# Kernel tuning notes

Hardware: AMD Instinct MI355X
Metric: run time of the kernel (lower is better)

The kernel has to match this reference:

```python
import jax, jax.numpy as jnp
import numpy as np

H, T, E = 8, 2048, 512


def setup_inputs() -> dict:
    key = jax.random.key(0)
    ks = jax.random.split(key, 11)
    s_e = 1.0 / np.sqrt(E)
    s_f = 1.0 / np.sqrt(H * T)
    return {
        "x": jax.random.normal(ks[0], (T, E), jnp.float32),
        "y": jax.random.normal(ks[1], (T, E), jnp.float32),
        "z": jax.random.normal(ks[2], (T, E), jnp.float32),
        "Wq": jax.random.normal(ks[3], (H, E, E), jnp.float32) * s_e,
        "bq": jax.random.normal(ks[4], (H, E), jnp.float32) * s_e,
        "Wk": jax.random.normal(ks[5], (H, E, E), jnp.float32) * s_e,
        "bk": jax.random.normal(ks[6], (H, E), jnp.float32) * s_e,
        "Wv": jax.random.normal(ks[7], (H, E, E), jnp.float32) * s_e,
        "bv": jax.random.normal(ks[8], (H, E), jnp.float32) * s_e,
        "Wf": jax.random.normal(ks[9], (T, H * T), jnp.float32) * s_f,
        "bf": jax.random.normal(ks[10], (T,), jnp.float32) * s_f,
    }


def reference(x, y, z, Wq, bq, Wk, bk, Wv, bv, Wf, bf):
    # Per-head projections: torch Linear is x @ W.T + b, W is [out,in]
    q = jnp.einsum("se,hfe->hsf", x, Wq) + bq[:, None, :]  # [H,T,E]
    k = jnp.einsum("se,hfe->hsf", y, Wk) + bk[:, None, :]
    v = jnp.einsum("se,hfe->hsf", z, Wv) + bv[:, None, :]
    # Scores scaled by sqrt(num query rows) = sqrt(T), as in the source
    scores = jnp.einsum("hsf,htf->hst", q, k) / jnp.sqrt(jnp.asarray(T, x.dtype))
    att = jax.nn.softmax(scores, axis=-1)
    heads_out = jnp.einsum("hst,htf->hsf", att, v)  # [H,T,E]
    concat = heads_out.reshape(H * T, E)  # cat along dim 0
    # finalLinear applied to concat.T: [E, H*T] @ Wf.T -> [E, T], then transpose
    final = (concat.T @ Wf.T + bf).T  # [T, E]
    residual = final + z
    # Manual per-row LayerNorm: (x - mean) / sqrt(std^2 + 1e-4), population std
    mean = jnp.mean(residual, axis=1, keepdims=True)
    var = jnp.var(residual, axis=1, keepdims=True)
    return (residual - mean) / jnp.sqrt(var + 1e-4)
```

## Files before the change

### kernel.cpp

```cpp
#include <hip/hip_runtime.h>
#include <hip/hip_bf16.h>
#include <cstdint>


#define HH 8
#define TT 2048
#define EE 512
#define HT (HH * TT)
#define HE (HH * EE)

typedef __bf16 bf16_t;
typedef __attribute__((ext_vector_type(8))) __bf16 bf16x8;
typedef __attribute__((ext_vector_type(4))) float f32x4;

__device__ __forceinline__ void gld_lds16(const bf16_t* __restrict__ g, bf16_t* l) {
  __builtin_amdgcn_global_load_lds(
      (const __attribute__((address_space(1))) unsigned int*)g,
      (__attribute__((address_space(3))) unsigned int*)l, 16, 0, 0);
}

__device__ __forceinline__ bf16x8 cvt8(float4 u, float4 v) {
  bf16x8 o;
  o[0] = (__bf16)u.x; o[1] = (__bf16)u.y; o[2] = (__bf16)u.z; o[3] = (__bf16)u.w;
  o[4] = (__bf16)v.x; o[5] = (__bf16)v.y; o[6] = (__bf16)v.z; o[7] = (__bf16)v.w;
  return o;
}

#define XCD_SWIZZLE()                                                              \
  const int gx = gridDim.x, gy = gridDim.y;                                        \
  const int nwg = gx * gy * (int)gridDim.z;                                        \
  const int lin = blockIdx.x + gx * (blockIdx.y + gy * blockIdx.z);                \
  const int qn_ = nwg >> 3, rn_ = nwg & 7;                                         \
  const int xcd_ = lin & 7, sub_ = lin >> 3;                                       \
  const int wgid =                                                                 \
      (xcd_ < rn_ ? xcd_ * (qn_ + 1) : rn_ * (qn_ + 1) + (xcd_ - rn_) * qn_) + sub_; \
  const int bx = wgid % gx;                                                        \
  const int t1_ = wgid / gx;                                                       \
  const int by = t1_ % gy;                                                         \
  const int z = t1_ / gy;

template <typename CT>
__global__ __launch_bounds__(512, 2) void gemm256_8ph(
    const bf16_t* __restrict__ A, const bf16_t* __restrict__ B, CT* __restrict__ C,
    const float* __restrict__ bias_n,
    int K, int lda, int ldb, int ldc,
    int64_t sA, int64_t sB, int64_t sC, int64_t sBN) {
  XCD_SWIZZLE();
  A += z * sA;
  B += z * sB;
  C += z * sC;
  if (bias_n) bias_n += z * sBN;

  const int m0 = bx * 256;
  const int n0 = by * 256;
  const int tid = threadIdx.x;

  __shared__ bf16_t lds[65536];
  bf16_t* sAl = lds;
  bf16_t* sBl = lds + 32768;

  const int srow = tid >> 3;
  const int csw = ((tid & 7) ^ (srow & 7)) * 8;
  const bf16_t* aS = A + (int64_t)(m0 + srow) * lda + csw;
  const bf16_t* bS = B + (int64_t)(n0 + srow) * ldb + csw;
  const int64_t l64a = (int64_t)64 * lda, l64b = (int64_t)64 * ldb;

  const int wave = tid >> 6, lane = tid & 63;
  const int wr = wave >> 2, wc = wave & 3;
  const int fr = lane & 15, qd = lane >> 4;
  const int aoff = wr * 8192 + fr * 64;
  const int boff = wc * 4096 + fr * 64;
  const int ck0 = ((0 * 4 + qd) ^ (fr & 7)) * 8;
  const int ck1 = ((1 * 4 + qd) ^ (fr & 7)) * 8;

  f32x4 acc[8][4];
#pragma unroll
  for (int i = 0; i < 8; i++)
#pragma unroll
    for (int j = 0; j < 4; j++) acc[i][j] = (f32x4){0.f, 0.f, 0.f, 0.f};

  bf16x8 aR[2][8];
  bf16x8 bR[2][2];

#define STG_A(d, h, t)                                                        \
  do {                                                                        \
    const bf16_t* g_ = aS + (int64_t)(h) * 128 * lda + (int64_t)(t) * 64;     \
    gld_lds16(g_, &sAl[(d) * 16384 + (h) * 8192 + tid * 8]);                  \
    gld_lds16(g_ + l64a, &sAl[(d) * 16384 + (h) * 8192 + 4096 + tid * 8]);    \
  } while (0)
#define STG_B(d, h, t)                                                        \
  do {                                                                        \
    const bf16_t* g_ = bS + (int64_t)(h) * 128 * ldb + (int64_t)(t) * 64;     \
    gld_lds16(g_, &sBl[(d) * 16384 + (h) * 8192 + tid * 8]);                  \
    gld_lds16(g_ + l64b, &sBl[(d) * 16384 + (h) * 8192 + 4096 + tid * 8]);    \
  } while (0)
#define RD_A(d, ih)                                                           \
  _Pragma("unroll") for (int i_ = 0; i_ < 4; i_++) {                          \
    const int b_ = (d) * 16384 + aoff + ((ih) * 4 + i_) * 1024;               \
    aR[0][(ih) * 4 + i_] = *(const bf16x8*)&sAl[b_ + ck0];                    \
    aR[1][(ih) * 4 + i_] = *(const bf16x8*)&sAl[b_ + ck1];                    \
  }
#define RD_B(d, jh)                                                           \
  _Pragma("unroll") for (int j_ = 0; j_ < 2; j_++) {                          \
    const int b_ = (d) * 16384 + boff + ((jh) * 2 + j_) * 1024;               \
    bR[0][j_] = *(const bf16x8*)&sBl[b_ + ck0];                               \
    bR[1][j_] = *(const bf16x8*)&sBl[b_ + ck1];                               \
  }
#define MM(qm, qn)                                                            \
  do {                                                                        \
    __builtin_amdgcn_s_setprio(1);                                            \
    _Pragma("unroll") for (int ks = 0; ks < 2; ks++)                          \
        _Pragma("unroll") for (int i_ = 0; i_ < 4; i_++)                      \
            _Pragma("unroll") for (int j_ = 0; j_ < 2; j_++)                  \
                acc[(qm) * 4 + i_][(qn) * 2 + j_] =                           \
                    __builtin_amdgcn_mfma_f32_16x16x32_bf16(                  \
                        aR[ks][(qm) * 4 + i_], bR[ks][j_],                    \
                        acc[(qm) * 4 + i_][(qn) * 2 + j_], 0, 0, 0);          \
    __builtin_amdgcn_s_setprio(0);                                            \
  } while (0)
#define BAR __builtin_amdgcn_s_barrier()
#define LGKM0                                                                 \
  do {                                                                        \
    asm volatile("s_waitcnt lgkmcnt(0)" ::: "memory");                        \
    __builtin_amdgcn_sched_barrier(0);                                        \
  } while (0)
#define VMC(n)                                                                \
  do {                                                                        \
    asm volatile("s_waitcnt vmcnt(" #n ")" ::: "memory");                     \
    __builtin_amdgcn_sched_barrier(0);                                        \
  } while (0)

  const int NT = K >> 6;

  STG_A(0, 0, 0); STG_A(0, 1, 0); STG_B(0, 0, 0); STG_B(0, 1, 0);
  STG_A(1, 0, 1); STG_A(1, 1, 1);
  VMC(4);
  BAR;

  for (int t0 = 0; t0 < NT; t0 += 2) {
    const int t1 = t0 + 1;
    const bool m2 = (t0 + 2) < NT;
    RD_A(0, 0); RD_B(0, 0);
    STG_B(1, 0, t1);
    BAR; LGKM0; MM(0, 0); BAR;
    RD_A(0, 1);
    STG_B(1, 1, t1);
    BAR; LGKM0; MM(1, 0); BAR;
    RD_B(0, 1);
    if (m2) STG_A(0, 0, t0 + 2);
    BAR; LGKM0; MM(0, 1); BAR;
    if (m2) STG_A(0, 1, t0 + 2);
    BAR; MM(1, 1);
    if (m2) { VMC(4); } else { VMC(0); }
    BAR;
    RD_A(1, 0); RD_B(1, 0);
    if (m2) STG_B(0, 0, t0 + 2);
    BAR; LGKM0; MM(0, 0); BAR;
    RD_A(1, 1);
    if (m2) STG_B(0, 1, t0 + 2);
    BAR; LGKM0; MM(1, 0); BAR;
    RD_B(1, 1);
    if (m2) STG_A(1, 0, t1 + 2);
    BAR; LGKM0; MM(0, 1); BAR;
    if (m2) STG_A(1, 1, t1 + 2);
    BAR; MM(1, 1);
    if (m2) VMC(4);
    BAR;
  }

#undef STG_A
#undef STG_B
#undef RD_A
#undef RD_B
#undef MM
#undef BAR
#undef LGKM0
#undef VMC

#pragma unroll
  for (int i = 0; i < 8; i++) {
    const int row0 = m0 + wr * 128 + i * 16 + qd * 4;
#pragma unroll
    for (int j = 0; j < 4; j++) {
      const int col = n0 + wc * 64 + j * 16 + fr;
      const float bn = bias_n ? bias_n[col] : 0.f;
#pragma unroll
      for (int r = 0; r < 4; r++)
        C[(int64_t)(row0 + r) * ldc + col] = (CT)(acc[i][j][r] + bn);
    }
  }
}

template <typename AT, typename CT>
__global__ __launch_bounds__(512, 4) void mfma_gemm_nt(
    const AT* __restrict__ A, const bf16_t* __restrict__ B, CT* __restrict__ C,
    const float* __restrict__ bias_m, const float* __restrict__ bias_n,
    int K, int lda, int ldb, int ldc,
    int64_t sA, int64_t sB, int64_t sC, int64_t sBM, int64_t sBN) {
  XCD_SWIZZLE();
  A += z * sA;
  B += z * sB;
  C += z * sC;
  if (bias_m) bias_m += z * sBM;
  if (bias_n) bias_n += z * sBN;

  const int m0 = bx * 128;
  const int n0 = by * 128;
  const int tid = threadIdx.x;

  __shared__ bf16_t sAb[2][128 * 64];
  __shared__ bf16_t sBb[2][128 * 64];

  const int srow = tid >> 3;
  const int sc = tid & 7;
  const int csw = (sc ^ (srow & 7)) * 8;
  const AT* a0 = A + (int64_t)(m0 + srow) * lda + csw;
  const AT* a1 = a0 + (int64_t)64 * lda;
  const bf16_t* b0 = B + (int64_t)(n0 + srow) * ldb + csw;
  const bf16_t* b1 = b0 + (int64_t)64 * ldb;

  const int wave = tid >> 6;
  const int lane = tid & 63;
  const int wm = (wave >> 2) * 64;
  const int wn = (wave & 3) * 32;
  const int fr = lane & 15;
  const int qd = lane >> 4;
  const int cx0 = ((0 * 4 + qd) ^ (fr & 7)) * 8;
  const int cx1 = ((1 * 4 + qd) ^ (fr & 7)) * 8;

  f32x4 acc[4][2];
#pragma unroll
  for (int i = 0; i < 4; i++)
#pragma unroll
    for (int j = 0; j < 2; j++) acc[i][j] = (f32x4){0.f, 0.f, 0.f, 0.f};

  float4 pa[4];

#define STAGE_B(buf, kt)                              \
  do {                                                \
    gld_lds16(b0 + (kt), &sBb[buf][tid * 8]);         \
    gld_lds16(b1 + (kt), &sBb[buf][4096 + tid * 8]);  \
  } while (0)
#define STAGE_A_BF16(buf, kt)                         \
  do {                                                \
    gld_lds16(a0 + (kt), &sAb[buf][tid * 8]);         \
    gld_lds16(a1 + (kt), &sAb[buf][4096 + tid * 8]);  \
  } while (0)
#define LOAD_A_F32(kt)                                \
  do {                                                \
    pa[0] = ((const float4*)(a0 + (kt)))[0];          \
    pa[1] = ((const float4*)(a0 + (kt)))[1];          \
    pa[2] = ((const float4*)(a1 + (kt)))[0];          \
    pa[3] = ((const float4*)(a1 + (kt)))[1];          \
  } while (0)
#define WRITE_A_F32(buf)                                      \
  do {                                                        \
    *(bf16x8*)&sAb[buf][tid * 8] = cvt8(pa[0], pa[1]);        \
    *(bf16x8*)&sAb[buf][4096 + tid * 8] = cvt8(pa[2], pa[3]); \
  } while (0)
#define COMPUTE(buf)                                                                   \
  do {                                                                                 \
    bf16x8 af[2][4], bfr[2][2];                                                        \
    _Pragma("unroll") for (int i = 0; i < 4; i++) {                                    \
      const int ar = (wm + i * 16 + fr) * 64;                                          \
      af[0][i] = *(const bf16x8*)&sAb[buf][ar + cx0];                                  \
      af[1][i] = *(const bf16x8*)&sAb[buf][ar + cx1];                                  \
    }                                                                                  \
    _Pragma("unroll") for (int j = 0; j < 2; j++) {                                    \
      const int br = (wn + j * 16 + fr) * 64;                                          \
      bfr[0][j] = *(const bf16x8*)&sBb[buf][br + cx0];                                 \
      bfr[1][j] = *(const bf16x8*)&sBb[buf][br + cx1];                                 \
    }                                                                                  \
    _Pragma("unroll") for (int ks = 0; ks < 2; ks++)                                   \
        _Pragma("unroll") for (int i = 0; i < 4; i++)                                  \
            _Pragma("unroll") for (int j = 0; j < 2; j++)                              \
                acc[i][j] = __builtin_amdgcn_mfma_f32_16x16x32_bf16(                   \
                    af[ks][i], bfr[ks][j], acc[i][j], 0, 0, 0);                        \
  } while (0)

  if constexpr (sizeof(AT) == 2) {
    STAGE_A_BF16(0, 0);
  } else {
    LOAD_A_F32(0);
    WRITE_A_F32(0);
  }
  STAGE_B(0, 0);
  __syncthreads();

  for (int kt = 0; kt < K; kt += 128) {
    if constexpr (sizeof(AT) == 2) {
      STAGE_A_BF16(1, kt + 64);
    } else {
      LOAD_A_F32(kt + 64);
    }
    STAGE_B(1, kt + 64);
    COMPUTE(0);
    if constexpr (sizeof(AT) == 4) WRITE_A_F32(1);
    __syncthreads();

    const bool more = (kt + 128) < K;
    if (more) {
      if constexpr (sizeof(AT) == 2) {
        STAGE_A_BF16(0, kt + 128);
      } else {
        LOAD_A_F32(kt + 128);
      }
      STAGE_B(0, kt + 128);
    }
    COMPUTE(1);
    if constexpr (sizeof(AT) == 4) {
      if (more) WRITE_A_F32(0);
    }
    __syncthreads();
  }

#undef STAGE_B
#undef STAGE_A_BF16
#undef LOAD_A_F32
#undef WRITE_A_F32
#undef COMPUTE

#pragma unroll
  for (int i = 0; i < 4; i++) {
    const int row0 = m0 + wm + i * 16 + qd * 4;
#pragma unroll
    for (int j = 0; j < 2; j++) {
      const int col = n0 + wn + j * 16 + fr;
      const float bn = bias_n ? bias_n[col] : 0.f;
#pragma unroll
      for (int r = 0; r < 4; r++) {
        const float bm = bias_m ? bias_m[row0 + r] : 0.f;
        C[(int64_t)(row0 + r) * ldc + col] = (CT)(acc[i][j][r] + bn + bm);
      }
    }
  }
}

__global__ __launch_bounds__(256) void fused_cvt(
    const float* __restrict__ x, const float* __restrict__ y,
    const float* __restrict__ z, const float* __restrict__ Wq,
    const float* __restrict__ Wk, const float* __restrict__ Wv,
    bf16_t* __restrict__ xb, bf16_t* __restrict__ yb, bf16_t* __restrict__ zb,
    bf16_t* __restrict__ Wqb, bf16_t* __restrict__ Wkb, bf16_t* __restrict__ Wvb) {
  const int b = blockIdx.x;
  const float* s;
  bf16_t* d;
  int off;
  if (b < 512) { s = x; d = xb; off = b; }
  else if (b < 1024) { s = y; d = yb; off = b - 512; }
  else if (b < 1536) { s = z; d = zb; off = b - 1024; }
  else if (b < 2560) { s = Wq; d = Wqb; off = b - 1536; }
  else if (b < 3584) { s = Wk; d = Wkb; off = b - 2560; }
  else { s = Wv; d = Wvb; off = b - 3584; }
  const int64_t i = ((int64_t)off * 256 + threadIdx.x) * 8;
  float4 u = ((const float4*)(s + i))[0];
  float4 v = ((const float4*)(s + i))[1];
  *(bf16x8*)(d + i) = cvt8(u, v);
}

__global__ __launch_bounds__(256) void softmax_rows(bf16_t* __restrict__ S) {
  const float scale = 0.022097086912079608f;
  bf16_t* p = S + (int64_t)blockIdx.x * TT;
  const int tid = threadIdx.x;
  bf16x8 in = *(const bf16x8*)(p + tid * 8);
  float v[8];
  float mx = -1e30f;
#pragma unroll
  for (int i = 0; i < 8; i++) {
    v[i] = (float)in[i] * scale;
    mx = fmaxf(mx, v[i]);
  }
#pragma unroll
  for (int o = 32; o > 0; o >>= 1) mx = fmaxf(mx, __shfl_xor(mx, o));
  __shared__ float redm[4], reds[4];
  if ((tid & 63) == 0) redm[tid >> 6] = mx;
  __syncthreads();
  mx = fmaxf(fmaxf(redm[0], redm[1]), fmaxf(redm[2], redm[3]));
  float sum = 0.f;
#pragma unroll
  for (int i = 0; i < 8; i++) {
    v[i] = __expf(v[i] - mx);
    sum += v[i];
  }
#pragma unroll
  for (int o = 32; o > 0; o >>= 1) sum += __shfl_xor(sum, o);
  if ((tid & 63) == 0) reds[tid >> 6] = sum;
  __syncthreads();
  sum = reds[0] + reds[1] + reds[2] + reds[3];
  const float inv = 1.0f / sum;
  bf16x8 o8;
#pragma unroll
  for (int i = 0; i < 8; i++) o8[i] = (__bf16)(v[i] * inv);
  *(bf16x8*)(p + tid * 8) = o8;
}

__global__ __launch_bounds__(256) void ln_res(const float* __restrict__ F,
                                              const float* __restrict__ Z,
                                              const float* __restrict__ BF,
                                              float* __restrict__ O, int np) {
  const int row = blockIdx.x;
  const int tid = threadIdx.x;
  const int64_t off = (int64_t)row * EE + tid;
  float a = 0.f, b = 0.f;
  for (int pz = 0; pz < np; pz++) {
    const float* f = F + (int64_t)pz * TT * EE;
    a += f[off];
    b += f[off + 256];
  }
  const float bft = BF[row];
  a += bft + Z[off];
  b += bft + Z[off + 256];
  float s = a + b, ss = a * a + b * b;
#pragma unroll
  for (int w = 32; w > 0; w >>= 1) {
    s += __shfl_xor(s, w);
    ss += __shfl_xor(ss, w);
  }
  __shared__ float rs[4], rss[4];
  if ((tid & 63) == 0) {
    rs[tid >> 6] = s;
    rss[tid >> 6] = ss;
  }
  __syncthreads();
  s = rs[0] + rs[1] + rs[2] + rs[3];
  ss = rss[0] + rss[1] + rss[2] + rss[3];
  const float mean = s * (1.0f / EE);
  const float var = ss * (1.0f / EE) - mean * mean;
  const float inv = rsqrtf(var + 1e-4f);
  float* o = O + (int64_t)row * EE;
  o[tid] = (a - mean) * inv;
  o[tid + 256] = (b - mean) * inv;
}

extern "C" void kernel_launch(void* const* d_in, const int* in_sizes, int n_in,
                              void* d_out, int out_size, void* d_ws, size_t ws_size,
                              hipStream_t stream) {
  const float* x = (const float*)d_in[0];
  const float* y = (const float*)d_in[1];
  const float* z = (const float*)d_in[2];
  const float* Wq = (const float*)d_in[3];
  const float* bq = (const float*)d_in[4];
  const float* Wk = (const float*)d_in[5];
  const float* bk = (const float*)d_in[6];
  const float* Wv = (const float*)d_in[7];
  const float* bv = (const float*)d_in[8];
  const float* Wf = (const float*)d_in[9];
  const float* bfb = (const float*)d_in[10];
  float* out = (float*)d_out;

  const size_t MB = 1ull << 20;
  char* p = (char*)d_ws;

  if (ws_size >= 151 * MB) {
    bf16_t* xb = (bf16_t*)(p + 0 * MB);
    bf16_t* yb = (bf16_t*)(p + 2 * MB);
    bf16_t* zb = (bf16_t*)(p + 4 * MB);
    bf16_t* Wqb = (bf16_t*)(p + 6 * MB);
    bf16_t* Wkb = (bf16_t*)(p + 10 * MB);
    bf16_t* Wvb = (bf16_t*)(p + 14 * MB);
    bf16_t* q = (bf16_t*)(p + 18 * MB);
    bf16_t* k = (bf16_t*)(p + 34 * MB);
    bf16_t* vT = (bf16_t*)(p + 50 * MB);
    bf16_t* att = (bf16_t*)(p + 66 * MB);
    bf16_t* hoT = (bf16_t*)(p + 130 * MB);
    float* finp = (float*)(p + 66 * MB);

    fused_cvt<<<4608, 256, 0, stream>>>(x, y, z, Wq, Wk, Wv, xb, yb, zb, Wqb, Wkb, Wvb);

    mfma_gemm_nt<bf16_t, bf16_t><<<dim3(16, 32, 1), 512, 0, stream>>>(
        xb, Wqb, q, nullptr, bq, EE, EE, EE, HE, 0, 0, 0, 0, 0);
    mfma_gemm_nt<bf16_t, bf16_t><<<dim3(16, 32, 1), 512, 0, stream>>>(
        yb, Wkb, k, nullptr, bk, EE, EE, EE, HE, 0, 0, 0, 0, 0);
    mfma_gemm_nt<bf16_t, bf16_t><<<dim3(32, 16, 1), 512, 0, stream>>>(
        Wvb, zb, vT, bv, nullptr, EE, EE, EE, TT, 0, 0, 0, 0, 0);
    gemm256_8ph<bf16_t><<<dim3(8, 8, 8), 512, 0, stream>>>(
        q, k, att, nullptr, EE, HE, HE, TT, EE, EE, (int64_t)TT * TT, 0);
    softmax_rows<<<HH * TT, 256, 0, stream>>>(att);
    mfma_gemm_nt<bf16_t, bf16_t><<<dim3(4, 16, 8), 512, 0, stream>>>(
        vT, att, hoT, nullptr, nullptr, TT, TT, TT, HT, (int64_t)EE * TT, (int64_t)TT * TT,
        (int64_t)TT, 0, 0);
    mfma_gemm_nt<float, float><<<dim3(16, 4, 8), 512, 0, stream>>>(
        Wf, hoT, finp, nullptr, nullptr, HT / 8, HT, HT, EE, HT / 8, HT / 8,
        (int64_t)TT * EE, 0, 0);
    ln_res<<<TT, 256, 0, stream>>>(finp, z, bfb, out, 8);
  } else {
    bf16_t* xb = (bf16_t*)(p + 0 * MB);
    bf16_t* yb = (bf16_t*)(p + 2 * MB);
    bf16_t* zb = (bf16_t*)(p + 4 * MB);
    bf16_t* Wqb = (bf16_t*)(p + 6 * MB);
    bf16_t* Wkb = (bf16_t*)(p + 10 * MB);
    bf16_t* Wvb = (bf16_t*)(p + 14 * MB);
    bf16_t* qh = (bf16_t*)(p + 18 * MB);
    bf16_t* kh = (bf16_t*)(p + 20 * MB);
    bf16_t* vTh = (bf16_t*)(p + 22 * MB);
    bf16_t* att = (bf16_t*)(p + 24 * MB);
    bf16_t* hoT = (bf16_t*)(p + 32 * MB);
    float* finp = (float*)(p + 0 * MB);

    fused_cvt<<<4608, 256, 0, stream>>>(x, y, z, Wq, Wk, Wv, xb, yb, zb, Wqb, Wkb, Wvb);

    for (int h = 0; h < HH; h++) {
      const bf16_t* Wq_h = Wqb + (int64_t)h * EE * EE;
      const bf16_t* Wk_h = Wkb + (int64_t)h * EE * EE;
      const bf16_t* Wv_h = Wvb + (int64_t)h * EE * EE;
      mfma_gemm_nt<bf16_t, bf16_t><<<dim3(16, 4, 1), 512, 0, stream>>>(
          xb, Wq_h, qh, nullptr, bq + h * EE, EE, EE, EE, EE, 0, 0, 0, 0, 0);
      mfma_gemm_nt<bf16_t, bf16_t><<<dim3(16, 4, 1), 512, 0, stream>>>(
          yb, Wk_h, kh, nullptr, bk + h * EE, EE, EE, EE, EE, 0, 0, 0, 0, 0);
      mfma_gemm_nt<bf16_t, bf16_t><<<dim3(4, 16, 1), 512, 0, stream>>>(
          Wv_h, zb, vTh, bv + h * EE, nullptr, EE, EE, EE, TT, 0, 0, 0, 0, 0);
      mfma_gemm_nt<bf16_t, bf16_t><<<dim3(16, 16, 1), 512, 0, stream>>>(
          qh, kh, att, nullptr, nullptr, EE, EE, EE, TT, 0, 0, 0, 0, 0);
      softmax_rows<<<TT, 256, 0, stream>>>(att);
      mfma_gemm_nt<bf16_t, bf16_t><<<dim3(4, 16, 1), 512, 0, stream>>>(
          vTh, att, hoT + (int64_t)h * TT, nullptr, nullptr, TT, TT, TT, HT, 0, 0, 0, 0, 0);
    }
    mfma_gemm_nt<float, float><<<dim3(16, 4, 8), 512, 0, stream>>>(
        Wf, hoT, finp, nullptr, nullptr, HT / 8, HT, HT, EE, HT / 8, HT / 8,
        (int64_t)TT * EE, 0, 0);
    ln_res<<<TT, 256, 0, stream>>>(finp, z, bfb, out, 8);
  }
}
```

Measured before the change: 428.3 us.

## Add fp32-A bf16-B k32 GEMM for final linear with 16-way split-K

Replaces the generic mfma_gemm_nt for the final linear with a dedicated kernel. It loads fp32 Wf rows from global memory, converts them to bf16 in registers, stages hoT via direct global-to-LDS loads, and double-buffers 32-wide K tiles. In the main path, split-K goes from 8 to 16 partitions to launch more blocks for this long-K GEMM. This adds more partial outputs for ln_res to sum and more fp32 partial traffic.

```diff
diff --git a/kernel.cpp b/kernel.cpp
--- a/kernel.cpp
+++ b/kernel.cpp
@@ -336,6 +336,102 @@
   }
 }
 
+__global__ __launch_bounds__(512, 8) void gemm_f32a_k32(
+    const float* __restrict__ A, const bf16_t* __restrict__ B, float* __restrict__ C,
+    int K, int lda, int ldb, int ldc, int64_t sA, int64_t sB, int64_t sC) {
+  XCD_SWIZZLE();
+  A += z * sA;
+  B += z * sB;
+  C += z * sC;
+
+  const int m0 = bx * 128;
+  const int n0 = by * 128;
+  const int tid = threadIdx.x;
+
+  __shared__ bf16_t sAb[2][128 * 32];
+  __shared__ bf16_t sBb[2][128 * 32];
+
+  const int srow = tid >> 2;
+  const int csw = ((tid & 3) ^ (srow & 3)) * 8;
+  const float* a0 = A + (int64_t)(m0 + srow) * lda + csw;
+  const bf16_t* b0 = B + (int64_t)(n0 + srow) * ldb + csw;
+
+  const int wave = tid >> 6;
+  const int lane = tid & 63;
+  const int wm = (wave >> 2) * 64;
+  const int wn = (wave & 3) * 32;
+  const int fr = lane & 15;
+  const int qd = lane >> 4;
+  const int ck = (qd ^ (fr & 3)) * 8;
+
+  f32x4 acc[4][2];
+#pragma unroll
+  for (int i = 0; i < 4; i++)
+#pragma unroll
+    for (int j = 0; j < 2; j++) acc[i][j] = (f32x4){0.f, 0.f, 0.f, 0.f};
+
+  float4 pa[2];
+
+#define STAGE_B32(buf, kt) gld_lds16(b0 + (kt), &sBb[buf][tid * 8])
+#define LOAD_A32(kt)                                \
+  do {                                              \
+    pa[0] = ((const float4*)(a0 + (kt)))[0];        \
+    pa[1] = ((const float4*)(a0 + (kt)))[1];        \
+  } while (0)
+#define WRITE_A32(buf) *(bf16x8*)&sAb[buf][tid * 8] = cvt8(pa[0], pa[1])
+#define COMPUTE32(buf)                                                                 \
+  do {                                                                                 \
+    bf16x8 af[4], bfr[2];                                                              \
+    _Pragma("unroll") for (int i = 0; i < 4; i++)                                      \
+        af[i] = *(const bf16x8*)&sAb[buf][(wm + i * 16 + fr) * 32 + ck];               \
+    _Pragma("unroll") for (int j = 0; j < 2; j++)                                      \
+        bfr[j] = *(const bf16x8*)&sBb[buf][(wn + j * 16 + fr) * 32 + ck];              \
+    _Pragma("unroll") for (int i = 0; i < 4; i++)                                      \
+        _Pragma("unroll") for (int j = 0; j < 2; j++)                                  \
+            acc[i][j] = __builtin_amdgcn_mfma_f32_16x16x32_bf16(                       \
+                af[i], bfr[j], acc[i][j], 0, 0, 0);                                    \
+  } while (0)
+
+  LOAD_A32(0);
+  WRITE_A32(0);
+  STAGE_B32(0, 0);
+  __syncthreads();
+
+  for (int kt = 0; kt < K; kt += 64) {
+    LOAD_A32(kt + 32);
+    STAGE_B32(1, kt + 32);
+    COMPUTE32(0);
+    WRITE_A32(1);
+    __syncthreads();
+
+    const bool more = (kt + 64) < K;
+    if (more) {
+      LOAD_A32(kt + 64);
+      STAGE_B32(0, kt + 64);
+    }
+    COMPUTE32(1);
+    if (more) WRITE_A32(0);
+    __syncthreads();
+  }
+
+#undef STAGE_B32
+#undef LOAD_A32
+#undef WRITE_A32
+#undef COMPUTE32
+
+#pragma unroll
+  for (int i = 0; i < 4; i++) {
+    const int row0 = m0 + wm + i * 16 + qd * 4;
+#pragma unroll
+    for (int j = 0; j < 2; j++) {
+      const int col = n0 + wn + j * 16 + fr;
+#pragma unroll
+      for (int r = 0; r < 4; r++)
+        C[(int64_t)(row0 + r) * ldc + col] = acc[i][j][r];
+    }
+  }
+}
+
 __global__ __launch_bounds__(256) void fused_cvt(
     const float* __restrict__ x, const float* __restrict__ y,
     const float* __restrict__ z, const float* __restrict__ Wq,
@@ -479,10 +575,9 @@
     mfma_gemm_nt<bf16_t, bf16_t><<<dim3(4, 16, 8), 512, 0, stream>>>(
         vT, att, hoT, nullptr, nullptr, TT, TT, TT, HT, (int64_t)EE * TT, (int64_t)TT * TT,
         (int64_t)TT, 0, 0);
-    mfma_gemm_nt<float, float><<<dim3(16, 4, 8), 512, 0, stream>>>(
-        Wf, hoT, finp, nullptr, nullptr, HT / 8, HT, HT, EE, HT / 8, HT / 8,
-        (int64_t)TT * EE, 0, 0);
-    ln_res<<<TT, 256, 0, stream>>>(finp, z, bfb, out, 8);
+    gemm_f32a_k32<<<dim3(16, 4, 16), 512, 0, stream>>>(
+        Wf, hoT, finp, HT / 16, HT, HT, EE, HT / 16, HT / 16, (int64_t)TT * EE);
+    ln_res<<<TT, 256, 0, stream>>>(finp, z, bfb, out, 16);
   } else {
     bf16_t* xb = (bf16_t*)(p + 0 * MB);
     bf16_t* yb = (bf16_t*)(p + 2 * MB);
@@ -515,9 +610,8 @@
       mfma_gemm_nt<bf16_t, bf16_t><<<dim3(4, 16, 1), 512, 0, stream>>>(
           vTh, att, hoT + (int64_t)h * TT, nullptr, nullptr, TT, TT, TT, HT, 0, 0, 0, 0, 0);
     }
-    mfma_gemm_nt<float, float><<<dim3(16, 4, 8), 512, 0, stream>>>(
-        Wf, hoT, finp, nullptr, nullptr, HT / 8, HT, HT, EE, HT / 8, HT / 8,
-        (int64_t)TT * EE, 0, 0);
+    gemm_f32a_k32<<<dim3(16, 4, 8), 512, 0, stream>>>(
+        Wf, hoT, finp, HT / 8, HT, HT, EE, HT / 8, HT / 8, (int64_t)TT * EE);
     ln_res<<<TT, 256, 0, stream>>>(finp, z, bfb, out, 8);
   }
 }
```

Measured after the change: 452.1 us. +5.6%, slower.
